# Kernel tuning notes

Hardware: AMD Instinct MI355X
Metric: run time of the kernel (lower is better)

## Reference

```python
import jax, jax.numpy as jnp
import numpy as np

B, T, C, H = 4, 2048, 1024, 16


def setup_inputs() -> dict:
    key = jax.random.key(0)
    ks = jax.random.split(key, 8)
    s = 0.02
    return {
        "xq": jax.random.normal(ks[0], (B, T, C), jnp.float32),
        "xk": jax.random.normal(ks[1], (B, T, C), jnp.float32),
        "xv": jax.random.normal(ks[2], (B, T, C), jnp.float32),
        "Wq": jax.random.normal(ks[3], (C, C), jnp.float32) * s,
        "Wk": jax.random.normal(ks[4], (C, C), jnp.float32) * s,
        "Wv": jax.random.normal(ks[5], (C, C), jnp.float32) * s,
        "Wo": jax.random.normal(ks[6], (C, C), jnp.float32) * s,
        "bo": jnp.zeros((C,), jnp.float32),
    }


def reference(xq, xk, xv, Wq, Wk, Wv, Wo, bo):
    # torch nn.Linear: y = x @ W.T
    q = xq @ Wq.T  # (B,T,C)
    k = xk @ Wk.T
    v = xv @ Wv.T
    hd = C // H
    # (B,T,C) -> (B,H,T,hd)
    q = q.reshape(B, T, H, hd).transpose(0, 2, 1, 3)
    k = k.reshape(B, T, H, hd).transpose(0, 2, 1, 3)
    v = v.reshape(B, T, H, hd).transpose(0, 2, 1, 3)
    scale = 1.0 / jnp.sqrt(jnp.asarray(hd, q.dtype))
    att = jnp.einsum("bhqd,bhkd->bhqk", q, k) * scale  # (B,H,T,T)
    causal = jnp.tril(jnp.ones((T, T), bool))
    att = jnp.where(causal, att, jnp.asarray(-jnp.inf, att.dtype))
    att = jax.nn.softmax(att, axis=-1)
    y = jnp.einsum("bhqk,bhkd->bhqd", att, v)  # (B,H,T,hd)
    y = y.transpose(0, 2, 1, 3).reshape(B, T, C)
    return y @ Wo.T + bo
```

## Files before the change

### kernel.cpp

```cpp
#include <hip/hip_runtime.h>
#include <stdint.h>

#define B_ 4
#define T_ 2048
#define C_ 1024
#define H_ 16
#define HD 64

typedef __attribute__((ext_vector_type(8))) short bf16x8;
typedef __attribute__((ext_vector_type(4))) short bf16x4;
typedef __attribute__((ext_vector_type(4))) float v4f;
typedef __attribute__((ext_vector_type(4))) uint32_t v4u;

static __device__ __forceinline__ short f2bf(float f) {
    union { float f; uint32_t u; } v; v.f = f;
    uint32_t u = v.u;
    uint32_t r = (u + 0x7fffu + ((u >> 16) & 1u)) >> 16;
    return (short)(r & 0xffffu);
}
static __device__ __forceinline__ uint32_t pack2(float x, float y) {
    uint32_t a = __float_as_uint(x) + 0x8000u;
    uint32_t b = __float_as_uint(y) + 0x8000u;
    return __builtin_amdgcn_perm(b, a, 0x07060302u);
}
static __device__ __forceinline__ uint32_t pack2t(float x, float y) {
    return __builtin_amdgcn_perm(__float_as_uint(y), __float_as_uint(x), 0x07060302u);
}
static __device__ __forceinline__ void gload_lds16(const void* g, void* l) {
    __builtin_amdgcn_global_load_lds(
        (const __attribute__((address_space(1))) void*)g,
        (__attribute__((address_space(3))) void*)l, 16, 0, 0);
}

__global__ __launch_bounds__(256) void convx(
    const float* __restrict__ x0, const float* __restrict__ x1,
    short* __restrict__ o0, short* __restrict__ o1,
    const float* __restrict__ w0, const float* __restrict__ w1,
    const float* __restrict__ w2, const float* __restrict__ w3,
    short* __restrict__ wout)
{
    int bid = blockIdx.x;
    const float* src; short* dst; size_t id;
    if (bid < 8192) {
        src = (bid < 4096) ? x0 : x1;
        dst = (bid < 4096) ? o0 : o1;
        id = (size_t)(bid & 4095) * 256 + threadIdx.x;
    } else {
        int wb = bid - 8192;
        int wi = wb >> 9;
        src = (wi == 0) ? w0 : (wi == 1) ? w1 : (wi == 2) ? w2 : w3;
        dst = wout + (size_t)wi * (C_ * C_);
        id = (size_t)(wb & 511) * 256 + threadIdx.x;
    }
    const float* p = src + id * 8;
    v4f a0 = *(const v4f*)p, a1 = *(const v4f*)(p + 4);
    v4u dv;
    dv[0] = pack2(a0[0], a0[1]); dv[1] = pack2(a0[2], a0[3]);
    dv[2] = pack2(a1[0], a1[1]); dv[3] = pack2(a1[2], a1[3]);
    *(v4u*)&dst[id * 8] = dv;
}


__global__ __launch_bounds__(256) void proj_gemm(
    const short* __restrict__ Xq, const short* __restrict__ Xk,
    const short* __restrict__ Wb, const float* __restrict__ xv,
    short* __restrict__ Qh, short* __restrict__ Kh, short* __restrict__ Vt,
    float qscale)
{
    const int K = 1024;
    __shared__ short As[128 * 32];
    __shared__ short Bs[128 * 32];
    const int t = threadIdx.x;
    const int w = t >> 6, l = t & 63, g = l >> 4, c = l & 15;
    const int wm = w & 1, wn = w >> 1;
    const int z = blockIdx.z;
    const int m0 = (z == 2 ? blockIdx.y : blockIdx.x) * 128;
    const int n0 = (z == 2 ? blockIdx.x : blockIdx.y) * 128;
    const short* Ab = (z == 0) ? Xq : (z == 1) ? Xk : (Wb + 2 * C_ * C_);
    const short* Bb = (z == 0) ? Wb : (Wb + C_ * C_);

    const int srow = l >> 2;
    const int sch = (l & 3) ^ ((l >> 3) & 3);
    const int gs = (g ^ ((c >> 1) & 3)) * 8;

    v4f acc[4][4];
#pragma unroll
    for (int i = 0; i < 4; ++i)
#pragma unroll
        for (int j = 0; j < 4; ++j) acc[i][j] = (v4f){0.f, 0.f, 0.f, 0.f};

    for (int k0 = 0; k0 < K; k0 += 32) {
        __syncthreads();
#pragma unroll
        for (int i = 0; i < 2; ++i) {
            int cb = w * 2 + i;
            gload_lds16(Ab + (size_t)(m0 + cb * 16 + srow) * K + k0 + sch * 8,
                        &As[cb * 512]);
        }
        if (z < 2) {
#pragma unroll
            for (int i = 0; i < 2; ++i) {
                int cb = w * 2 + i;
                gload_lds16(Bb + (size_t)(n0 + cb * 16 + srow) * K + k0 + sch * 8,
                            &Bs[cb * 512]);
            }
        } else {
#pragma unroll
            for (int i = 0; i < 2; ++i) {
                int id = i * 256 + t;
                int rr = id >> 2, cc = id & 3;
                const float* p = xv + (size_t)(n0 + rr) * K + k0 + cc * 8;
                v4f a0 = *(const v4f*)p, a1 = *(const v4f*)(p + 4);
                v4u dv;
                dv[0] = pack2(a0[0], a0[1]); dv[1] = pack2(a0[2], a0[3]);
                dv[2] = pack2(a1[0], a1[1]); dv[3] = pack2(a1[2], a1[3]);
                *(v4u*)&Bs[rr * 32 + ((cc ^ ((rr >> 1) & 3)) * 8)] = dv;
            }
        }
        __syncthreads();
        bf16x8 af[4], bfr[4];
#pragma unroll
        for (int i = 0; i < 4; ++i)
            af[i] = *(const bf16x8*)&As[(wm * 64 + i * 16 + c) * 32 + gs];
#pragma unroll
        for (int j = 0; j < 4; ++j)
            bfr[j] = *(const bf16x8*)&Bs[(wn * 64 + j * 16 + c) * 32 + gs];
#pragma unroll
        for (int i = 0; i < 4; ++i)
#pragma unroll
            for (int j = 0; j < 4; ++j)
                acc[i][j] = __builtin_amdgcn_mfma_f32_16x16x32_bf16(af[i], bfr[j], acc[i][j], 0, 0, 0);
    }
    if (z < 2) {
        short* Out = (z == 0) ? Qh : Kh;
        const float os = (z == 0) ? qscale : 1.0f;
#pragma unroll
        for (int i = 0; i < 4; ++i)
#pragma unroll
            for (int j = 0; j < 4; ++j)
#pragma unroll
                for (int r = 0; r < 4; ++r) {
                    int m = m0 + wm * 64 + i * 16 + g * 4 + r;
                    int n = n0 + wn * 64 + j * 16 + c;
                    int b = m >> 11, tt = m & (T_ - 1);
                    int h = n >> 6, d = n & 63;
                    Out[((size_t)(b * H_ + h) * T_ + tt) * HD + d] = f2bf(acc[i][j][r] * os);
                }
    } else {
#pragma unroll
        for (int i = 0; i < 4; ++i)
#pragma unroll
            for (int j = 0; j < 4; ++j)
#pragma unroll
                for (int r = 0; r < 4; ++r) {
                    int m = m0 + wm * 64 + i * 16 + g * 4 + r;
                    int n = n0 + wn * 64 + j * 16 + c;
                    int b = n >> 11, tt = n & (T_ - 1);
                    int h = m >> 6, d = m & 63;
                    Vt[((size_t)(b * H_ + h) * HD + d) * T_ + tt] = f2bf(acc[i][j][r]);
                }
    }
}

__global__ __launch_bounds__(256) void gemm_o(
    const short* __restrict__ Yb, const short* __restrict__ Wo,
    float* __restrict__ Out, const float* __restrict__ bias)
{
    const int K = 1024;
    __shared__ short As[128 * 32];
    __shared__ short Bs[128 * 32];
    const int t = threadIdx.x;
    const int w = t >> 6, l = t & 63, g = l >> 4, c = l & 15;
    const int wm = w & 1, wn = w >> 1;
    const int m0 = blockIdx.x * 128, n0 = blockIdx.y * 128;

    const int srow = l >> 2;
    const int sch = (l & 3) ^ ((l >> 3) & 3);
    const int gs = (g ^ ((c >> 1) & 3)) * 8;

    v4f acc[4][4];
#pragma unroll
    for (int i = 0; i < 4; ++i)
#pragma unroll
        for (int j = 0; j < 4; ++j) acc[i][j] = (v4f){0.f, 0.f, 0.f, 0.f};

    for (int k0 = 0; k0 < K; k0 += 32) {
        __syncthreads();
#pragma unroll
        for (int i = 0; i < 2; ++i) {
            int cb = w * 2 + i;
            gload_lds16(Yb + (size_t)(m0 + cb * 16 + srow) * K + k0 + sch * 8,
                        &As[cb * 512]);
            gload_lds16(Wo + (size_t)(n0 + cb * 16 + srow) * K + k0 + sch * 8,
                        &Bs[cb * 512]);
        }
        __syncthreads();
        bf16x8 af[4], bfr[4];
#pragma unroll
        for (int i = 0; i < 4; ++i)
            af[i] = *(const bf16x8*)&As[(wm * 64 + i * 16 + c) * 32 + gs];
#pragma unroll
        for (int j = 0; j < 4; ++j)
            bfr[j] = *(const bf16x8*)&Bs[(wn * 64 + j * 16 + c) * 32 + gs];
#pragma unroll
        for (int i = 0; i < 4; ++i)
#pragma unroll
            for (int j = 0; j < 4; ++j)
                acc[i][j] = __builtin_amdgcn_mfma_f32_16x16x32_bf16(af[i], bfr[j], acc[i][j], 0, 0, 0);
    }
#pragma unroll
    for (int i = 0; i < 4; ++i)
#pragma unroll
        for (int j = 0; j < 4; ++j)
#pragma unroll
            for (int r = 0; r < 4; ++r) {
                int m = m0 + wm * 64 + i * 16 + g * 4 + r;
                int n = n0 + wn * 64 + j * 16 + c;
                Out[(size_t)m * C_ + n] = acc[i][j][r] + bias[n];
            }
}

__global__ __launch_bounds__(256) void attn_kernel(
    const short* __restrict__ Q, const short* __restrict__ Kp,
    const short* __restrict__ Vt, short* __restrict__ Y)
{
    __shared__ short Ks[2 * 64 * 32];
    __shared__ short Vs[64 * 72];
    const int t = threadIdx.x;
    const int w = t >> 6, l = t & 63, g = l >> 4, c = l & 15;
    const int bid = blockIdx.x;
    const int slot = bid >> 3;
    const int p = slot & 15;
    const size_t bh = (size_t)((bid & 7) * 8 + (slot >> 4));

    const int srow = l >> 2;
    const int sch = (l & 3) ^ ((l >> 3) & 3);
    const int gs = (g ^ ((c >> 1) & 3)) * 8;

    bf16x8 ones;
#pragma unroll
    for (int i = 0; i < 8; ++i) ones[i] = (short)0x3F80;

    for (int qi = 0; qi < 2; ++qi) {
        const int qt = qi ? (31 - p) : p;
        const int qbase = qt * 64;

        bf16x8 qf0, qf1;
        {
            const short* qp = &Q[(bh * T_ + qbase + w * 16 + c) * HD + g * 8];
            qf0 = *(const bf16x8*)qp;
            qf1 = *(const bf16x8*)(qp + 32);
        }

        v4f O[4], accl;
        accl = (v4f){0.f, 0.f, 0.f, 0.f};
#pragma unroll
        for (int d = 0; d < 4; ++d) O[d] = (v4f){0.f, 0.f, 0.f, 0.f};

        for (int kb = 0; kb <= qt; ++kb) {
            const int kbase = kb * 64;
            __syncthreads();
#pragma unroll
            for (int i = 0; i < 2; ++i) {
                int gi = w * 2 + i;
                int hk = gi >> 2, rb = gi & 3;
                const short* gp = &Kp[(bh * T_ + kbase + rb * 16 + srow) * HD + hk * 32 + sch * 8];
                gload_lds16(gp, &Ks[hk * 2048 + rb * 512]);
            }
#pragma unroll
            for (int i = 0; i < 2; ++i) {
                int id = i * 256 + t;
                int rr = id >> 3, cc = id & 7;
                *(bf16x8*)&Vs[rr * 72 + cc * 8] =
                    *(const bf16x8*)&Vt[(bh * HD + rr) * T_ + kbase + cc * 8];
            }
            __syncthreads();

            float s2[4][4];
#pragma unroll
            for (int j = 0; j < 4; ++j) {
                bf16x8 kf0 = *(const bf16x8*)&Ks[(j * 16 + c) * 32 + gs];
                bf16x8 kf1 = *(const bf16x8*)&Ks[2048 + (j * 16 + c) * 32 + gs];
                v4f sa = (v4f){0.f, 0.f, 0.f, 0.f};
                sa = __builtin_amdgcn_mfma_f32_16x16x32_bf16(kf0, qf0, sa, 0, 0, 0);
                sa = __builtin_amdgcn_mfma_f32_16x16x32_bf16(kf1, qf1, sa, 0, 0, 0);
#pragma unroll
                for (int r = 0; r < 4; ++r) s2[j][r] = sa[r];
            }
            if (kb == qt) {
                const int q = qbase + w * 16 + c;
#pragma unroll
                for (int j = 0; j < 4; ++j)
#pragma unroll
                    for (int r = 0; r < 4; ++r) {
                        int key = kbase + j * 16 + g * 4 + r;
                        if (key > q) s2[j][r] = -3.0e38f;
                    }
            }
            union { bf16x8 v; uint32_t u[4]; } pa[2];
#pragma unroll
            for (int s = 0; s < 2; ++s)
#pragma unroll
                for (int wi = 0; wi < 4; ++wi) {
                    int j = 2 * s + (wi >> 1);
                    int r0 = (wi & 1) * 2;
                    float x = __builtin_amdgcn_exp2f(s2[j][r0]);
                    float y = __builtin_amdgcn_exp2f(s2[j][r0 + 1]);
                    pa[s].u[wi] = pack2t(x, y);
                }
#pragma unroll
            for (int s = 0; s < 2; ++s) {
                bf16x8 af = pa[s].v;
#pragma unroll
                for (int d = 0; d < 4; ++d) {
                    const short* vp = &Vs[(d * 16 + c) * 72 + s * 32 + g * 4];
                    union { bf16x8 v8; bf16x4 v4[2]; } vu;
                    vu.v4[0] = *(const bf16x4*)vp;
                    vu.v4[1] = *(const bf16x4*)(vp + 16);
                    O[d] = __builtin_amdgcn_mfma_f32_16x16x32_bf16(af, vu.v8, O[d], 0, 0, 0);
                }
                accl = __builtin_amdgcn_mfma_f32_16x16x32_bf16(af, ones, accl, 0, 0, 0);
            }
        }
#pragma unroll
        for (int r = 0; r < 4; ++r) {
            float rl = 1.0f / accl[r];
            size_t rowoff = ((size_t)(bh >> 4) * T_ + qbase + w * 16 + g * 4 + r) * C_ + (bh & 15) * HD;
#pragma unroll
            for (int d = 0; d < 4; ++d)
                Y[rowoff + d * 16 + c] = f2bf(O[d][r] * rl);
        }
    }
}

extern "C" void kernel_launch(void* const* d_in, const int* in_sizes, int n_in,
                              void* d_out, int out_size, void* d_ws, size_t ws_size,
                              hipStream_t stream) {
    const float* xq = (const float*)d_in[0];
    const float* xk = (const float*)d_in[1];
    const float* xv = (const float*)d_in[2];
    const float* Wq = (const float*)d_in[3];
    const float* Wk = (const float*)d_in[4];
    const float* Wv = (const float*)d_in[5];
    const float* Wo = (const float*)d_in[6];
    const float* bo = (const float*)d_in[7];

    const size_t NE = (size_t)B_ * H_ * T_ * HD;
    const size_t WE = (size_t)C_ * C_;
    short* Qh    = (short*)d_ws;
    short* Kh    = Qh + NE;
    short* slotA = Kh + NE;
    short* slotB = slotA + NE;
    short* Wbf   = slotB + NE;
    short* Vt    = (short*)d_out;

    const float qscale = 0.18033688011112042f;
    dim3 blk(256);

    hipLaunchKernelGGL(convx, dim3(10240), blk, 0, stream,
                       xq, xk, slotA, slotB, Wq, Wk, Wv, Wo, Wbf);
    hipLaunchKernelGGL(proj_gemm, dim3(64, 8, 3), blk, 0, stream,
                       slotA, slotB, Wbf, xv, Qh, Kh, Vt, qscale);
    hipLaunchKernelGGL(attn_kernel, dim3(B_ * H_ * (T_ / 128)), blk, 0, stream,
                       Qh, Kh, Vt, slotA);
    hipLaunchKernelGGL(gemm_o, dim3(64, 8), blk, 0, stream,
                       slotA, Wbf + 3 * WE, (float*)d_out, bo);
}
```

Before: 323.5 us.

## Double-buffer LDS tiles in projection, output GEMM and attention kernels

Adds a second LDS buffer to the projection GEMM, the output GEMM and the attention kernel. The next K/V or A/B tile is prefetched while MFMAs run on the current one, and the xv and V register loads are stored to LDS after compute. This drops one barrier per iteration and is meant to hide global-load latency behind matrix math. In exchange it doubles LDS use, which may lower occupancy, and raises register pressure from the prefetch registers.

```diff
diff --git a/kernel.cpp b/kernel.cpp
--- a/kernel.cpp
+++ b/kernel.cpp
@@ -61,6 +61,7 @@
 }
 
 
+
 __global__ __launch_bounds__(256) void proj_gemm(
     const short* __restrict__ Xq, const short* __restrict__ Xk,
     const short* __restrict__ Wb, const float* __restrict__ xv,
@@ -68,8 +69,8 @@
     float qscale)
 {
     const int K = 1024;
-    __shared__ short As[128 * 32];
-    __shared__ short Bs[128 * 32];
+    __shared__ short As[2][128 * 32];
+    __shared__ short Bs[2][128 * 32];
     const int t = threadIdx.x;
     const int w = t >> 6, l = t & 63, g = l >> 4, c = l & 15;
     const int wm = w & 1, wn = w >> 1;
@@ -89,47 +90,88 @@
 #pragma unroll
         for (int j = 0; j < 4; ++j) acc[i][j] = (v4f){0.f, 0.f, 0.f, 0.f};
 
-    for (int k0 = 0; k0 < K; k0 += 32) {
-        __syncthreads();
+#pragma unroll
+    for (int i = 0; i < 2; ++i) {
+        int cb = w * 2 + i;
+        gload_lds16(Ab + (size_t)(m0 + cb * 16 + srow) * K + sch * 8, &As[0][cb * 512]);
+    }
+    if (z < 2) {
 #pragma unroll
         for (int i = 0; i < 2; ++i) {
             int cb = w * 2 + i;
-            gload_lds16(Ab + (size_t)(m0 + cb * 16 + srow) * K + k0 + sch * 8,
-                        &As[cb * 512]);
-        }
-        if (z < 2) {
+            gload_lds16(Bb + (size_t)(n0 + cb * 16 + srow) * K + sch * 8, &Bs[0][cb * 512]);
+        }
+    } else {
+#pragma unroll
+        for (int i = 0; i < 2; ++i) {
+            int id = i * 256 + t;
+            int rr = id >> 2, cc = id & 3;
+            const float* p = xv + (size_t)(n0 + rr) * K + cc * 8;
+            v4f a0 = *(const v4f*)p, a1 = *(const v4f*)(p + 4);
+            v4u dv;
+            dv[0] = pack2(a0[0], a0[1]); dv[1] = pack2(a0[2], a0[3]);
+            dv[2] = pack2(a1[0], a1[1]); dv[3] = pack2(a1[2], a1[3]);
+            *(v4u*)&Bs[0][rr * 32 + ((cc ^ ((rr >> 1) & 3)) * 8)] = dv;
+        }
+    }
+    __syncthreads();
+
+    int cur = 0;
+    for (int k0 = 0; k0 < K; k0 += 32) {
+        const int nxt = cur ^ 1;
+        const int kn = k0 + 32;
+        const bool pre = (kn < K);
+        v4f pb0[2], pb1[2];
+        if (pre) {
 #pragma unroll
             for (int i = 0; i < 2; ++i) {
                 int cb = w * 2 + i;
-                gload_lds16(Bb + (size_t)(n0 + cb * 16 + srow) * K + k0 + sch * 8,
-                            &Bs[cb * 512]);
-            }
-        } else {
+                gload_lds16(Ab + (size_t)(m0 + cb * 16 + srow) * K + kn + sch * 8,
+                            &As[nxt][cb * 512]);
+            }
+            if (z < 2) {
+#pragma unroll
+                for (int i = 0; i < 2; ++i) {
+                    int cb = w * 2 + i;
+                    gload_lds16(Bb + (size_t)(n0 + cb * 16 + srow) * K + kn + sch * 8,
+                                &Bs[nxt][cb * 512]);
+                }
+            } else {
+#pragma unroll
+                for (int i = 0; i < 2; ++i) {
+                    int id = i * 256 + t;
+                    int rr = id >> 2, cc = id & 3;
+                    const float* p = xv + (size_t)(n0 + rr) * K + kn + cc * 8;
+                    pb0[i] = *(const v4f*)p;
+                    pb1[i] = *(const v4f*)(p + 4);
+                }
+            }
+        }
+        bf16x8 af[4], bfr[4];
+#pragma unroll
+        for (int i = 0; i < 4; ++i)
+            af[i] = *(const bf16x8*)&As[cur][(wm * 64 + i * 16 + c) * 32 + gs];
+#pragma unroll
+        for (int j = 0; j < 4; ++j)
+            bfr[j] = *(const bf16x8*)&Bs[cur][(wn * 64 + j * 16 + c) * 32 + gs];
+#pragma unroll
+        for (int i = 0; i < 4; ++i)
+#pragma unroll
+            for (int j = 0; j < 4; ++j)
+                acc[i][j] = __builtin_amdgcn_mfma_f32_16x16x32_bf16(af[i], bfr[j], acc[i][j], 0, 0, 0);
+        if (pre && z == 2) {
 #pragma unroll
             for (int i = 0; i < 2; ++i) {
                 int id = i * 256 + t;
                 int rr = id >> 2, cc = id & 3;
-                const float* p = xv + (size_t)(n0 + rr) * K + k0 + cc * 8;
-                v4f a0 = *(const v4f*)p, a1 = *(const v4f*)(p + 4);
                 v4u dv;
-                dv[0] = pack2(a0[0], a0[1]); dv[1] = pack2(a0[2], a0[3]);
-                dv[2] = pack2(a1[0], a1[1]); dv[3] = pack2(a1[2], a1[3]);
-                *(v4u*)&Bs[rr * 32 + ((cc ^ ((rr >> 1) & 3)) * 8)] = dv;
+                dv[0] = pack2(pb0[i][0], pb0[i][1]); dv[1] = pack2(pb0[i][2], pb0[i][3]);
+                dv[2] = pack2(pb1[i][0], pb1[i][1]); dv[3] = pack2(pb1[i][2], pb1[i][3]);
+                *(v4u*)&Bs[nxt][rr * 32 + ((cc ^ ((rr >> 1) & 3)) * 8)] = dv;
             }
         }
         __syncthreads();
-        bf16x8 af[4], bfr[4];
-#pragma unroll
-        for (int i = 0; i < 4; ++i)
-            af[i] = *(const bf16x8*)&As[(wm * 64 + i * 16 + c) * 32 + gs];
-#pragma unroll
-        for (int j = 0; j < 4; ++j)
-            bfr[j] = *(const bf16x8*)&Bs[(wn * 64 + j * 16 + c) * 32 + gs];
-#pragma unroll
-        for (int i = 0; i < 4; ++i)
-#pragma unroll
-            for (int j = 0; j < 4; ++j)
-                acc[i][j] = __builtin_amdgcn_mfma_f32_16x16x32_bf16(af[i], bfr[j], acc[i][j], 0, 0, 0);
+        cur = nxt;
     }
     if (z < 2) {
         short* Out = (z == 0) ? Qh : Kh;
@@ -167,8 +209,8 @@
     float* __restrict__ Out, const float* __restrict__ bias)
 {
     const int K = 1024;
-    __shared__ short As[128 * 32];
-    __shared__ short Bs[128 * 32];
+    __shared__ short As[2][128 * 32];
+    __shared__ short Bs[2][128 * 32];
     const int t = threadIdx.x;
     const int w = t >> 6, l = t & 63, g = l >> 4, c = l & 15;
     const int wm = w & 1, wn = w >> 1;
@@ -184,29 +226,42 @@
 #pragma unroll
         for (int j = 0; j < 4; ++j) acc[i][j] = (v4f){0.f, 0.f, 0.f, 0.f};
 
+#pragma unroll
+    for (int i = 0; i < 2; ++i) {
+        int cb = w * 2 + i;
+        gload_lds16(Yb + (size_t)(m0 + cb * 16 + srow) * K + sch * 8, &As[0][cb * 512]);
+        gload_lds16(Wo + (size_t)(n0 + cb * 16 + srow) * K + sch * 8, &Bs[0][cb * 512]);
+    }
+    __syncthreads();
+
+    int cur = 0;
     for (int k0 = 0; k0 < K; k0 += 32) {
-        __syncthreads();
-#pragma unroll
-        for (int i = 0; i < 2; ++i) {
-            int cb = w * 2 + i;
-            gload_lds16(Yb + (size_t)(m0 + cb * 16 + srow) * K + k0 + sch * 8,
-                        &As[cb * 512]);
-            gload_lds16(Wo + (size_t)(n0 + cb * 16 + srow) * K + k0 + sch * 8,
-                        &Bs[cb * 512]);
-        }
-        __syncthreads();
+        const int nxt = cur ^ 1;
+        const int kn = k0 + 32;
+        if (kn < K) {
+#pragma unroll
+            for (int i = 0; i < 2; ++i) {
+                int cb = w * 2 + i;
+                gload_lds16(Yb + (size_t)(m0 + cb * 16 + srow) * K + kn + sch * 8,
+                            &As[nxt][cb * 512]);
+                gload_lds16(Wo + (size_t)(n0 + cb * 16 + srow) * K + kn + sch * 8,
+                            &Bs[nxt][cb * 512]);
+            }
+        }
         bf16x8 af[4], bfr[4];
 #pragma unroll
         for (int i = 0; i < 4; ++i)
-            af[i] = *(const bf16x8*)&As[(wm * 64 + i * 16 + c) * 32 + gs];
+            af[i] = *(const bf16x8*)&As[cur][(wm * 64 + i * 16 + c) * 32 + gs];
 #pragma unroll
         for (int j = 0; j < 4; ++j)
-            bfr[j] = *(const bf16x8*)&Bs[(wn * 64 + j * 16 + c) * 32 + gs];
+            bfr[j] = *(const bf16x8*)&Bs[cur][(wn * 64 + j * 16 + c) * 32 + gs];
 #pragma unroll
         for (int i = 0; i < 4; ++i)
 #pragma unroll
             for (int j = 0; j < 4; ++j)
                 acc[i][j] = __builtin_amdgcn_mfma_f32_16x16x32_bf16(af[i], bfr[j], acc[i][j], 0, 0, 0);
+        __syncthreads();
+        cur = nxt;
     }
 #pragma unroll
     for (int i = 0; i < 4; ++i)
@@ -224,8 +279,8 @@
     const short* __restrict__ Q, const short* __restrict__ Kp,
     const short* __restrict__ Vt, short* __restrict__ Y)
 {
-    __shared__ short Ks[2 * 64 * 32];
-    __shared__ short Vs[64 * 72];
+    __shared__ short Ks[2][2 * 64 * 32];
+    __shared__ short Vs[2][64 * 72];
     const int t = threadIdx.x;
     const int w = t >> 6, l = t & 63, g = l >> 4, c = l & 15;
     const int bid = blockIdx.x;
@@ -257,30 +312,50 @@
 #pragma unroll
         for (int d = 0; d < 4; ++d) O[d] = (v4f){0.f, 0.f, 0.f, 0.f};
 
+#pragma unroll
+        for (int i = 0; i < 2; ++i) {
+            int gi = w * 2 + i;
+            int hk = gi >> 2, rb = gi & 3;
+            gload_lds16(&Kp[(bh * T_ + rb * 16 + srow) * HD + hk * 32 + sch * 8],
+                        &Ks[0][hk * 2048 + rb * 512]);
+        }
+#pragma unroll
+        for (int i = 0; i < 2; ++i) {
+            int id = i * 256 + t;
+            int rr = id >> 3, cc = id & 7;
+            *(bf16x8*)&Vs[0][rr * 72 + cc * 8] =
+                *(const bf16x8*)&Vt[(bh * HD + rr) * T_ + cc * 8];
+        }
+        __syncthreads();
+
+        int cur = 0;
         for (int kb = 0; kb <= qt; ++kb) {
             const int kbase = kb * 64;
-            __syncthreads();
-#pragma unroll
-            for (int i = 0; i < 2; ++i) {
-                int gi = w * 2 + i;
-                int hk = gi >> 2, rb = gi & 3;
-                const short* gp = &Kp[(bh * T_ + kbase + rb * 16 + srow) * HD + hk * 32 + sch * 8];
-                gload_lds16(gp, &Ks[hk * 2048 + rb * 512]);
-            }
-#pragma unroll
-            for (int i = 0; i < 2; ++i) {
-                int id = i * 256 + t;
-                int rr = id >> 3, cc = id & 7;
-                *(bf16x8*)&Vs[rr * 72 + cc * 8] =
-                    *(const bf16x8*)&Vt[(bh * HD + rr) * T_ + kbase + cc * 8];
-            }
-            __syncthreads();
+            const int nxt = cur ^ 1;
+            const bool pre = (kb < qt);
+            bf16x8 vpre[2];
+            if (pre) {
+                const int kb2 = kbase + 64;
+#pragma unroll
+                for (int i = 0; i < 2; ++i) {
+                    int gi = w * 2 + i;
+                    int hk = gi >> 2, rb = gi & 3;
+                    gload_lds16(&Kp[(bh * T_ + kb2 + rb * 16 + srow) * HD + hk * 32 + sch * 8],
+                                &Ks[nxt][hk * 2048 + rb * 512]);
+                }
+#pragma unroll
+                for (int i = 0; i < 2; ++i) {
+                    int id = i * 256 + t;
+                    int rr = id >> 3, cc = id & 7;
+                    vpre[i] = *(const bf16x8*)&Vt[(bh * HD + rr) * T_ + kb2 + cc * 8];
+                }
+            }
 
             float s2[4][4];
 #pragma unroll
             for (int j = 0; j < 4; ++j) {
-                bf16x8 kf0 = *(const bf16x8*)&Ks[(j * 16 + c) * 32 + gs];
-                bf16x8 kf1 = *(const bf16x8*)&Ks[2048 + (j * 16 + c) * 32 + gs];
+                bf16x8 kf0 = *(const bf16x8*)&Ks[cur][(j * 16 + c) * 32 + gs];
+                bf16x8 kf1 = *(const bf16x8*)&Ks[cur][2048 + (j * 16 + c) * 32 + gs];
                 v4f sa = (v4f){0.f, 0.f, 0.f, 0.f};
                 sa = __builtin_amdgcn_mfma_f32_16x16x32_bf16(kf0, qf0, sa, 0, 0, 0);
                 sa = __builtin_amdgcn_mfma_f32_16x16x32_bf16(kf1, qf1, sa, 0, 0, 0);
@@ -313,7 +388,7 @@
                 bf16x8 af = pa[s].v;
 #pragma unroll
                 for (int d = 0; d < 4; ++d) {
-                    const short* vp = &Vs[(d * 16 + c) * 72 + s * 32 + g * 4];
+                    const short* vp = &Vs[cur][(d * 16 + c) * 72 + s * 32 + g * 4];
                     union { bf16x8 v8; bf16x4 v4[2]; } vu;
                     vu.v4[0] = *(const bf16x4*)vp;
                     vu.v4[1] = *(const bf16x4*)(vp + 16);
@@ -321,6 +396,17 @@
                 }
                 accl = __builtin_amdgcn_mfma_f32_16x16x32_bf16(af, ones, accl, 0, 0, 0);
             }
+
+            if (pre) {
+#pragma unroll
+                for (int i = 0; i < 2; ++i) {
+                    int id = i * 256 + t;
+                    int rr = id >> 3, cc = id & 7;
+                    *(bf16x8*)&Vs[nxt][rr * 72 + cc * 8] = vpre[i];
+                }
+            }
+            __syncthreads();
+            cur = nxt;
         }
 #pragma unroll
         for (int r = 0; r < 4; ++r) {
```

Result: no change. 329.4 us (+1.8%).
